# Performance work log

Measured on AMD Instinct MI355X. Metric: run time of the kernel, lower is better.

## Reference

```python
import jax, jax.numpy as jnp
import numpy as np

KSIZE = 7
FEAT_SIZE = 64
BETA = 0.02


def _resize_bilinear_ac(x, out_h, out_w):
    """Bilinear resize with align_corners=True. x: (B, C, H, W)."""
    H, W = x.shape[-2], x.shape[-1]
    ys = jnp.linspace(0.0, H - 1.0, out_h)
    xs = jnp.linspace(0.0, W - 1.0, out_w)
    y0 = jnp.clip(jnp.floor(ys).astype(jnp.int32), 0, H - 1)
    x0 = jnp.clip(jnp.floor(xs).astype(jnp.int32), 0, W - 1)
    y1 = jnp.minimum(y0 + 1, H - 1)
    x1 = jnp.minimum(x0 + 1, W - 1)
    wy = (ys - y0.astype(x.dtype))[None, None, :, None]
    wx = (xs - x0.astype(x.dtype))[None, None, None, :]
    rows = x[:, :, y0, :] * (1.0 - wy) + x[:, :, y1, :] * wy      # (B,C,out_h,W)
    out = rows[:, :, :, x0] * (1.0 - wx) + rows[:, :, :, x1] * wx  # (B,C,out_h,out_w)
    return out


def _sce(feat, w, b):
    """EfficientSpatialContextNet: shifted local-correlation context + 1x1 conv + relu."""
    B, C, h, wd = feat.shape
    k, pad = KSIZE, KSIZE // 2
    # F.normalize(p=2, dim=1) with eps=1e-12 (clamped norm)
    fn = feat / jnp.maximum(jnp.sqrt(jnp.sum(feat * feat, axis=1, keepdims=True)), 1e-12)
    fp = jnp.pad(fn, ((0, 0), (0, 0), (pad, pad), (pad, pad)))
    offsets = ([(i, i) for i in range(k)]
               + [(i, pad) for i in range(k)]
               + [(i, k - 1 - i) for i in range(k)]
               + [(pad, i) for i in range(k)])
    ctx = jnp.stack([jnp.sum(fp[:, :, r:h + r, c:wd + c] * fn, axis=1)
                     for (r, c) in offsets], axis=1)  # (B, 4k, h, w)
    out = jnp.concatenate([feat, ctx], axis=1)        # (B, C+4k, h, w)
    out = jnp.einsum('oc,bchw->bohw', w, out) + b[None, :, None, None]
    return jax.nn.relu(out)


def _l2norm(f):
    # FeatureL2Norm: eps added inside sqrt
    return f / jnp.sqrt(jnp.sum(f * f, axis=1, keepdims=True) + 1e-6)


def _forward(src_feat, tgt_feat, sce_w, sce_b):
    fs = FEAT_SIZE
    s = _l2norm(_sce(src_feat, sce_w, sce_b))
    t = _l2norm(_sce(tgt_feat, sce_w, sce_b))
    B, C, hs, ws = s.shape
    ht, wt = t.shape[2], t.shape[3]
    Ls, Lt = hs * ws, ht * wt
    corr = jnp.einsum('bcs,bct->bst', s.reshape(B, C, Ls), t.reshape(B, C, Lt))
    # mutual NN filter (Rocco et al.)
    smax = jnp.max(corr, axis=2, keepdims=True)
    tmax = jnp.max(corr, axis=1, keepdims=True)
    smax = jnp.where(smax == 0, 1e-30, smax)
    tmax = jnp.where(tmax == 0, 1e-30, tmax)
    corr = corr * ((corr / smax) * (corr / tmax))
    # resize corr on source grid, then on target grid (bilinear, align_corners=True)
    c_s2t = jnp.transpose(corr, (0, 2, 1)).reshape(B, Lt, hs, ws)
    c_s2t = _resize_bilinear_ac(c_s2t, fs, fs)                       # (B, Lt, fs, fs)
    c_t2s = jnp.transpose(c_s2t.reshape(B, Lt, fs * fs), (0, 2, 1)).reshape(B, fs * fs, ht, wt)
    c = _resize_bilinear_ac(c_t2s, fs, fs)                           # (B, fs*fs, fs, fs)
    # soft argmax with temperature (softmax over source positions)
    p = jax.nn.softmax(c / BETA, axis=1).reshape(B, fs, fs, fs, fs)  # (B, hs', ws', ht', wt')
    xn = jnp.linspace(-1.0, 1.0, fs).astype(c.dtype)
    yn = jnp.linspace(-1.0, 1.0, fs).astype(c.dtype)
    grid_x = jnp.einsum('bijhw,j->bhw', p, xn)
    grid_y = jnp.einsum('bijhw,i->bhw', p, yn)
    flow_norm = jnp.stack([grid_x, grid_y], axis=1)                  # (B, 2, fs, fs)
    # unnormalise mapping and convert to flow
    H = W = fs
    mx = (flow_norm[:, 0] + 1.0) * (W - 1) / 2.0
    my = (flow_norm[:, 1] + 1.0) * (H - 1) / 2.0
    xx = jnp.arange(W, dtype=flow_norm.dtype)[None, None, :]
    yy = jnp.arange(H, dtype=flow_norm.dtype)[None, :, None]
    flow = jnp.stack([mx - xx, my - yy], axis=1)                     # (B, 2, fs, fs)
    return flow


def setup_inputs() -> dict:
    key = jax.random.key(0)
    k1, k2, k3 = jax.random.split(key, 3)
    B, C, h, w = 4, 1024, 32, 32
    src_feat = jax.random.normal(k1, (B, C, h, w), dtype=jnp.float32)
    tgt_feat = jax.random.normal(k2, (B, C, h, w), dtype=jnp.float32)
    sce_w = jax.random.normal(k3, (2048, C + 4 * KSIZE), dtype=jnp.float32) * 0.03
    sce_b = jnp.zeros((2048,), dtype=jnp.float32)
    return {"src_feat": src_feat, "tgt_feat": tgt_feat, "sce_w": sce_w, "sce_b": sce_b}


def reference(src_feat, tgt_feat, sce_w, sce_b):
    return _forward(src_feat, tgt_feat, sce_w, sce_b)
```

## Files before the change

### kernel.cpp

```cpp
#include <hip/hip_runtime.h>
#include <math.h>

#define HW    1024
#define CIN   1024
#define CCTX  28
#define CALL  1052
#define COUT  2048
#define CCHNK 512

typedef _Float16 half8   __attribute__((ext_vector_type(8)));
typedef _Float16 half4_t __attribute__((ext_vector_type(4)));
typedef _Float16 half2_t __attribute__((ext_vector_type(2)));
typedef __fp16   fp16x2  __attribute__((ext_vector_type(2)));
typedef float    f32x4   __attribute__((ext_vector_type(4)));

__device__ __forceinline__ void split2(float a0, float a1, half2_t& h, half2_t& l) {
    float h0 = __uint_as_float(__float_as_uint(a0) & 0xFFFFE000u);
    float h1 = __uint_as_float(__float_as_uint(a1) & 0xFFFFE000u);
    fp16x2 hp = __builtin_amdgcn_cvt_pkrtz(h0, h1);
    fp16x2 lp = __builtin_amdgcn_cvt_pkrtz(a0 - h0, a1 - h1);
    h = __builtin_bit_cast(half2_t, hp);
    l = __builtin_bit_cast(half2_t, lp);
}
__device__ __forceinline__ void split4(float4 v, half4_t& h, half4_t& l) {
    half2_t ha, la, hb, lb;
    split2(v.x, v.y, ha, la);
    split2(v.z, v.w, hb, lb);
    h = __builtin_shufflevector(ha, hb, 0, 1, 2, 3);
    l = __builtin_shufflevector(la, lb, 0, 1, 2, 3);
}
__device__ __forceinline__ float f4get(const float4& v, int e) {
    return e == 0 ? v.x : e == 1 ? v.y : e == 2 ? v.z : v.w;
}

__global__ void pnorm_part(const float* __restrict__ src, const float* __restrict__ tgt,
                           float* __restrict__ parts) {
    int img = blockIdx.x, pb = blockIdx.y, part = blockIdx.z;
    int p = pb * 64 + threadIdx.x;
    const float* feat = ((img < 4) ? src + (size_t)img * CIN * HW
                                   : tgt + (size_t)(img - 4) * CIN * HW)
                        + (size_t)part * 256 * HW + p;
    float a4[4] = {};
    for (int c = 0; c < 256; c += 8) {
        float v[8];
#pragma unroll
        for (int j = 0; j < 8; ++j) v[j] = feat[(size_t)(c + j) * HW];
#pragma unroll
        for (int j = 0; j < 8; ++j) a4[j & 3] = fmaf(v[j], v[j], a4[j & 3]);
    }
    parts[(size_t)part * 8192 + img * 1024 + p] = (a4[0] + a4[1]) + (a4[2] + a4[3]);
}
__global__ void pnorm_combine(const float* __restrict__ parts, float* __restrict__ pnorm) {
    int img = blockIdx.x;
    int p = blockIdx.y * 64 + threadIdx.x;
    float s = parts[img * 1024 + p] + parts[8192 + img * 1024 + p]
            + parts[16384 + img * 1024 + p] + parts[24576 + img * 1024 + p];
    pnorm[img * HW + p] = fmaxf(sqrtf(s), 1e-12f);
}

__global__ void ctx_kernel(const float* __restrict__ src, const float* __restrict__ tgt,
                           const float* __restrict__ pnorm, float* __restrict__ ctx) {
    int img = blockIdx.x;
    int y = blockIdx.y;
    int tid = threadIdx.x;
    int o = tid >> 5;
    int x = tid & 31;
    const float* feat = (img < 4) ? src + (size_t)img * CIN * HW
                                  : tgt + (size_t)(img - 4) * CIN * HW;
    int g = o / 7, i = o % 7;
    int r, c;
    if (g == 0)      { r = i; c = i; }
    else if (g == 1) { r = i; c = 3; }
    else if (g == 2) { r = i; c = 6 - i; }
    else             { r = 3; c = i; }
    int y2 = y + r - 3, x2 = x + c - 3;
    int p = y * 32 + x;
    float outv = 0.f;
    if (y2 >= 0 && y2 < 32 && x2 >= 0 && x2 < 32) {
        int p2 = y2 * 32 + x2;
        const float* f0 = feat + p;
        const float* f1 = feat + p2;
        float acc = 0.f;
        for (int ch = 0; ch < CIN; ++ch)
            acc = fmaf(f0[(size_t)ch * HW], f1[(size_t)ch * HW], acc);
        outv = acc / (pnorm[img * HW + p] * pnorm[img * HW + p2]);
    }
    ctx[((size_t)img * CCTX + o) * HW + p] = outv;
}

template <bool FIRST>
__global__ __launch_bounds__(256) void conv_mfma(
    const float* __restrict__ src, const float* __restrict__ tgt,
    const float* __restrict__ ctxb, const float* __restrict__ w,
    const float* __restrict__ bias, _Float16* __restrict__ yh,
    _Float16* __restrict__ yl, float* __restrict__ nrm_parts, int c0) {
    __shared__ __align__(16) char smem[51200];
    _Float16* Ah = (_Float16*)smem;
    _Float16* Al = Ah + 2560;
    _Float16* Wh = Al + 2560;
    _Float16* Wl = Wh + 10240;

    int cb = blockIdx.x, pb = blockIdx.y, img = blockIdx.z;
    int n0 = pb * 64;
    int m0g = c0 + cb * 256;
    const float* feat = (img < 4) ? src + (size_t)img * CIN * HW
                                  : tgt + (size_t)(img - 4) * CIN * HW;
    const float* ctxi = ctxb + (size_t)img * CCTX * HW;
    int tid = threadIdx.x;
    int lane = tid & 63, wv = tid >> 6;
    int frow = lane & 15, kg = (lane >> 4) * 8;
    int aq = tid & 15, ar = tid >> 4;

    float4 xa[2], xw[8];
    auto stage_regs = [&](int k0) {
#pragma unroll
        for (int j = 0; j < 2; ++j) {
            int k = k0 + ar * 2 + j;
            if (k < CIN)       xa[j] = *(const float4*)(feat + (size_t)k * HW + n0 + aq * 4);
            else if (k < CALL) xa[j] = *(const float4*)(ctxi + (size_t)(k - CIN) * HW + n0 + aq * 4);
            else               xa[j] = make_float4(0.f, 0.f, 0.f, 0.f);
        }
#pragma unroll
        for (int i = 0; i < 8; ++i) {
            int k = k0 + i * 4;
            xw[i] = (k + 4 <= CALL) ? *(const float4*)(w + (size_t)(m0g + tid) * CALL + k)
                                    : make_float4(0.f, 0.f, 0.f, 0.f);
        }
    };
    auto write_lds = [&]() {
#pragma unroll
        for (int p = 0; p < 4; ++p) {
            half2_t h, l;
            split2(f4get(xa[0], p), f4get(xa[1], p), h, l);
            int row = aq * 4 + p;
            *(half2_t*)(Ah + row * 40 + ar * 2) = h;
            *(half2_t*)(Al + row * 40 + ar * 2) = l;
        }
#pragma unroll
        for (int i = 0; i < 8; ++i) {
            half4_t h, l;
            split4(xw[i], h, l);
            *(half4_t*)(Wh + tid * 40 + i * 4) = h;
            *(half4_t*)(Wl + tid * 40 + i * 4) = l;
        }
    };

    f32x4 acc[4][4] = {};
    const int NT = 33;
    stage_regs(0); write_lds();
    __syncthreads();
    for (int t = 0; t < NT; ++t) {
        half8 afh[4], afl[4], bfh[4], bfl[4];
#pragma unroll
        for (int fm = 0; fm < 4; ++fm) {
            int r = fm * 16 + frow;
            afh[fm] = *(const half8*)(Ah + r * 40 + kg);
            afl[fm] = *(const half8*)(Al + r * 40 + kg);
        }
#pragma unroll
        for (int fn = 0; fn < 4; ++fn) {
            int r = wv * 64 + fn * 16 + frow;
            bfh[fn] = *(const half8*)(Wh + r * 40 + kg);
            bfl[fn] = *(const half8*)(Wl + r * 40 + kg);
        }
        if (t + 1 < NT) stage_regs((t + 1) * 32);
#pragma unroll
        for (int fm = 0; fm < 4; ++fm)
#pragma unroll
            for (int fn = 0; fn < 4; ++fn) {
                acc[fm][fn] = __builtin_amdgcn_mfma_f32_16x16x32_f16(afh[fm], bfh[fn], acc[fm][fn], 0, 0, 0);
                acc[fm][fn] = __builtin_amdgcn_mfma_f32_16x16x32_f16(afh[fm], bfl[fn], acc[fm][fn], 0, 0, 0);
                acc[fm][fn] = __builtin_amdgcn_mfma_f32_16x16x32_f16(afl[fm], bfh[fn], acc[fm][fn], 0, 0, 0);
            }
        __syncthreads();
        if (t + 1 < NT) write_lds();
        __syncthreads();
    }

    float bv[4];
#pragma unroll
    for (int fn = 0; fn < 4; ++fn) bv[fn] = bias[m0g + wv * 64 + fn * 16 + frow];

    float* nsf = (float*)smem;
    _Float16* yb = (_Float16*)(smem + 2048);
    float psum[4][4] = {};
#pragma unroll
    for (int fm = 0; fm < 4; ++fm)
#pragma unroll
        for (int fn = 0; fn < 4; ++fn)
#pragma unroll
            for (int r = 0; r < 4; ++r) {
                float v = fmaxf(acc[fm][fn][r] + bv[fn], 0.f);
                acc[fm][fn][r] = v;
                psum[fm][r] = fmaf(v, v, psum[fm][r]);
            }
#pragma unroll
    for (int off = 1; off <= 8; off <<= 1)
#pragma unroll
        for (int fm = 0; fm < 4; ++fm)
#pragma unroll
            for (int r = 0; r < 4; ++r)
                psum[fm][r] = psum[fm][r] + __shfl_xor(psum[fm][r], off);
    if (frow == 0) {
#pragma unroll
        for (int fm = 0; fm < 4; ++fm)
#pragma unroll
            for (int r = 0; r < 4; ++r)
                nsf[wv * 64 + fm * 16 + (lane >> 4) * 4 + r] = psum[fm][r];
    }
    __syncthreads();
    float sv = 0.f;
    if (tid < 64)
        sv = nsf[tid] + nsf[64 + tid] + nsf[128 + tid] + nsf[192 + tid];
#pragma unroll
    for (int fm = 0; fm < 4; ++fm)
#pragma unroll
        for (int fn = 0; fn < 4; ++fn)
#pragma unroll
            for (int r = 0; r < 4; ++r) {
                float v = acc[fm][fn][r];
                float hf = __uint_as_float(__float_as_uint(v) & 0xFFFFE000u);
                int pix_l = fm * 16 + (lane >> 4) * 4 + r;
                int chan_l = wv * 64 + fn * 16 + frow;
                yb[pix_l * 264 + chan_l] = (_Float16)hf;
            }
    __syncthreads();
    {
        int row = tid >> 2, seg = tid & 3;
        _Float16* gp = yh + ((size_t)img * HW + n0 + row) * CCHNK + cb * 256 + seg * 64;
#pragma unroll
        for (int i = 0; i < 8; ++i)
            *(half8*)(gp + i * 8) = *(const half8*)(yb + row * 264 + seg * 64 + i * 8);
    }
    __syncthreads();
#pragma unroll
    for (int fm = 0; fm < 4; ++fm)
#pragma unroll
        for (int fn = 0; fn < 4; ++fn)
#pragma unroll
            for (int r = 0; r < 4; ++r) {
                float v = acc[fm][fn][r];
                float hf = __uint_as_float(__float_as_uint(v) & 0xFFFFE000u);
                int pix_l = fm * 16 + (lane >> 4) * 4 + r;
                int chan_l = wv * 64 + fn * 16 + frow;
                yb[pix_l * 264 + chan_l] = (_Float16)(v - hf);
            }
    __syncthreads();
    {
        int row = tid >> 2, seg = tid & 3;
        _Float16* gp = yl + ((size_t)img * HW + n0 + row) * CCHNK + cb * 256 + seg * 64;
#pragma unroll
        for (int i = 0; i < 8; ++i)
            *(half8*)(gp + i * 8) = *(const half8*)(yb + row * 264 + seg * 64 + i * 8);
    }
    if (tid < 64) {
        float* np = nrm_parts + ((size_t)img * 2 + cb) * HW + n0 + tid;
        if (FIRST) *np = sv; else *np += sv;
    }
}

template <int MODE>
__global__ __launch_bounds__(256) void corr_mfma(
    const _Float16* __restrict__ yh, const _Float16* __restrict__ yl,
    const float* __restrict__ nrm_sq, float* __restrict__ corrT,
    float* __restrict__ spar, float* __restrict__ tpar) {
    __shared__ float rm[2][128];
    __shared__ float cm[2][128];
    int sb = blockIdx.x, tb = blockIdx.y, b = blockIdx.z;
    int tid = threadIdx.x, lane = tid & 63, wv = tid >> 6;
    int wm = wv >> 1, wn = wv & 1;
    int frow = lane & 15, kg = (lane >> 4) * 8;

    size_t trow = (size_t)(4 + b) * HW + tb * 128 + wm * 64 + frow;
    size_t srow = (size_t)b * HW + sb * 128 + wn * 64 + frow;
    const _Float16* ahp = yh + trow * CCHNK + kg;
    const _Float16* alp = yl + trow * CCHNK + kg;
    const _Float16* bhp = yh + srow * CCHNK + kg;
    const _Float16* blp = yl + srow * CCHNK + kg;

    f32x4 acc[4][4] = {};
#pragma unroll 2
    for (int t = 0; t < 16; ++t) {
        int k0 = t * 32;
        half8 ah[4], al_[4], bh[4], bl[4];
#pragma unroll
        for (int f = 0; f < 4; ++f) {
            size_t ro = (size_t)f * 16 * CCHNK + k0;
            ah[f]  = *(const half8*)(ahp + ro);
            al_[f] = *(const half8*)(alp + ro);
            bh[f]  = *(const half8*)(bhp + ro);
            bl[f]  = *(const half8*)(blp + ro);
        }
#pragma unroll
        for (int fm = 0; fm < 4; ++fm)
#pragma unroll
            for (int fn = 0; fn < 4; ++fn) {
                acc[fm][fn] = __builtin_amdgcn_mfma_f32_16x16x32_f16(ah[fm],  bh[fn], acc[fm][fn], 0, 0, 0);
                acc[fm][fn] = __builtin_amdgcn_mfma_f32_16x16x32_f16(ah[fm],  bl[fn], acc[fm][fn], 0, 0, 0);
                acc[fm][fn] = __builtin_amdgcn_mfma_f32_16x16x32_f16(al_[fm], bh[fn], acc[fm][fn], 0, 0, 0);
            }
    }

    float rnt[4][4], rns[4];
    float rowmax[4][4] = {};
    float colmax[4] = {};
    if (MODE == 2) {
#pragma unroll
        for (int fm = 0; fm < 4; ++fm)
#pragma unroll
            for (int r = 0; r < 4; ++r) {
                int t = tb * 128 + wm * 64 + fm * 16 + (lane >> 4) * 4 + r;
                rnt[fm][r] = 1.f / sqrtf(nrm_sq[(size_t)(4 + b) * HW + t] + 1e-6f);
            }
#pragma unroll
        for (int fn = 0; fn < 4; ++fn) {
            int s_ = sb * 128 + wn * 64 + fn * 16 + frow;
            rns[fn] = 1.f / sqrtf(nrm_sq[(size_t)b * HW + s_] + 1e-6f);
        }
    }
#pragma unroll
    for (int fm = 0; fm < 4; ++fm)
#pragma unroll
        for (int r = 0; r < 4; ++r) {
            int t = tb * 128 + wm * 64 + fm * 16 + (lane >> 4) * 4 + r;
            float* cp = corrT + ((size_t)b * HW + t) * HW + sb * 128 + wn * 64 + frow;
#pragma unroll
            for (int fn = 0; fn < 4; ++fn) {
                float v = acc[fm][fn][r];
                if (MODE >= 1) v += cp[fn * 16];
                if (MODE == 2) {
                    v *= rnt[fm][r] * rns[fn];
                    rowmax[fm][r] = fmaxf(rowmax[fm][r], v);
                    colmax[fn] = fmaxf(colmax[fn], v);
                }
                cp[fn * 16] = v;
            }
        }
    if (MODE == 2) {
#pragma unroll
        for (int off = 1; off <= 8; off <<= 1)
#pragma unroll
            for (int fm = 0; fm < 4; ++fm)
#pragma unroll
                for (int r = 0; r < 4; ++r)
                    rowmax[fm][r] = fmaxf(rowmax[fm][r], __shfl_xor(rowmax[fm][r], off));
        if (frow == 0) {
#pragma unroll
            for (int fm = 0; fm < 4; ++fm)
#pragma unroll
                for (int r = 0; r < 4; ++r)
                    rm[wn][wm * 64 + fm * 16 + (lane >> 4) * 4 + r] = rowmax[fm][r];
        }
#pragma unroll
        for (int off = 16; off <= 32; off <<= 1)
#pragma unroll
            for (int fn = 0; fn < 4; ++fn)
                colmax[fn] = fmaxf(colmax[fn], __shfl_xor(colmax[fn], off));
        if (lane < 16) {
#pragma unroll
            for (int fn = 0; fn < 4; ++fn)
                cm[wm][wn * 64 + fn * 16 + lane] = colmax[fn];
        }
        __syncthreads();
        if (tid < 128)
            tpar[((size_t)b * 8 + sb) * HW + tb * 128 + tid] = fmaxf(rm[0][tid], rm[1][tid]);
        if (tid < 128)
            spar[((size_t)b * 8 + tb) * HW + sb * 128 + tid] = fmaxf(cm[0][tid], cm[1][tid]);
    }
}

__global__ void nrm_reduce(const float* __restrict__ nrm_parts, float* __restrict__ nrm_sq) {
    int img = blockIdx.y;
    int p = blockIdx.x * 256 + threadIdx.x;
    nrm_sq[img * HW + p] = nrm_parts[((size_t)img * 2 + 0) * HW + p]
                         + nrm_parts[((size_t)img * 2 + 1) * HW + p];
}

__global__ void combine_max(const float* __restrict__ spar, const float* __restrict__ tpar,
                            float* __restrict__ smax, float* __restrict__ tmax) {
    int b = blockIdx.y;
    int i = blockIdx.x * 256 + threadIdx.x;
    float m = 0.f;
#pragma unroll
    for (int q = 0; q < 8; ++q) m = fmaxf(m, spar[((size_t)b * 8 + q) * HW + i]);
    smax[b * HW + i] = m;
    float m2 = 0.f;
#pragma unroll
    for (int q = 0; q < 8; ++q) m2 = fmaxf(m2, tpar[((size_t)b * 8 + q) * HW + i]);
    tmax[b * HW + i] = m2;
}

__global__ __launch_bounds__(256) void final_kernel(const float* __restrict__ corrT,
                                                    const float* __restrict__ smax,
                                                    const float* __restrict__ tmax,
                                                    float* __restrict__ out) {
    __shared__ float vsh[1024];
    __shared__ float rbuf[16];
    int b = blockIdx.z;
    int typ = blockIdx.y;
    int txp = blockIdx.x;
    int tid = threadIdx.x;

    float fy = typ * (31.0f / 63.0f);
    int y0 = min((int)fy, 31); int y1 = min(y0 + 1, 31);
    float wy = fy - (float)y0;
    float fx = txp * (31.0f / 63.0f);
    int x0 = min((int)fx, 31); int x1 = min(x0 + 1, 31);
    float wx = fx - (float)x0;
    int tA = y0 * 32 + x0, tB = y0 * 32 + x1, tC = y1 * 32 + x0, tD = y1 * 32 + x1;
    const float* base = corrT + (size_t)b * HW * HW;
    const float* rA = base + (size_t)tA * HW;
    const float* rB = base + (size_t)tB * HW;
    const float* rC = base + (size_t)tC * HW;
    const float* rD = base + (size_t)tD * HW;
    float tmA_ = tmax[b * HW + tA]; if (tmA_ == 0.f) tmA_ = 1e-30f;
    float tmB_ = tmax[b * HW + tB]; if (tmB_ == 0.f) tmB_ = 1e-30f;
    float tmC_ = tmax[b * HW + tC]; if (tmC_ == 0.f) tmC_ = 1e-30f;
    float tmD_ = tmax[b * HW + tD]; if (tmD_ == 0.f) tmD_ = 1e-30f;
    float itA = 1.f / tmA_, itB = 1.f / tmB_, itC = 1.f / tmC_, itD = 1.f / tmD_;
    float wA = (1.f - wy) * (1.f - wx), wB = (1.f - wy) * wx;
    float wC = wy * (1.f - wx), wD = wy * wx;
#pragma unroll
    for (int u = 0; u < 4; ++u) {
        int s = u * 256 + tid;
        float sm = smax[b * HW + s]; if (sm == 0.f) sm = 1e-30f;
        float is = 1.f / sm;
        float a = rA[s]; a = a * a * a * is * itA;
        float b2 = rB[s]; b2 = b2 * b2 * b2 * is * itB;
        float c2 = rC[s]; c2 = c2 * c2 * c2 * is * itC;
        float d2 = rD[s]; d2 = d2 * d2 * d2 * is * itD;
        vsh[s] = wA * a + wB * b2 + wC * c2 + wD * d2;
    }
    __syncthreads();

    int jx = tid & 63;
    int wvq = tid >> 6;
    float gxx = jx * (31.0f / 63.0f);
    int sx0 = min((int)gxx, 31), sx1 = min(sx0 + 1, 31);
    float wxx = gxx - (float)sx0, iwxx = 1.f - wxx;
    float xnj = jx * (2.0f / 63.0f) - 1.0f;

    float cv[16];
    float lmax = -1e30f;
#pragma unroll
    for (int u = 0; u < 16; ++u) {
        int iy = u * 4 + wvq;
        float gy = iy * (31.0f / 63.0f);
        int sy0 = min((int)gy, 31), sy1 = min(sy0 + 1, 31);
        float wyy = gy - (float)sy0;
        float r0 = vsh[sy0 * 32 + sx0] * iwxx + vsh[sy0 * 32 + sx1] * wxx;
        float r1 = vsh[sy1 * 32 + sx0] * iwxx + vsh[sy1 * 32 + sx1] * wxx;
        cv[u] = (r0 * (1.f - wyy) + r1 * wyy) * 50.0f;
        lmax = fmaxf(lmax, cv[u]);
    }
#pragma unroll
    for (int off = 32; off >= 1; off >>= 1) lmax = fmaxf(lmax, __shfl_down(lmax, off));
    int lane = tid & 63;
    if (lane == 0) rbuf[wvq] = lmax;
    __syncthreads();
    if (tid == 0) {
        float m = rbuf[0];
        for (int i = 1; i < 4; ++i) m = fmaxf(m, rbuf[i]);
        rbuf[0] = m;
    }
    __syncthreads();
    float m = rbuf[0];

    float e0 = 0.f, ex = 0.f, ey = 0.f;
#pragma unroll
    for (int u = 0; u < 16; ++u) {
        int iy = u * 4 + wvq;
        float e = __expf(cv[u] - m);
        e0 += e;
        ex = fmaf(e, xnj, ex);
        ey = fmaf(e, iy * (2.0f / 63.0f) - 1.0f, ey);
    }
#pragma unroll
    for (int off = 32; off >= 1; off >>= 1) {
        e0 += __shfl_down(e0, off);
        ex += __shfl_down(ex, off);
        ey += __shfl_down(ey, off);
    }
    if (lane == 0) { rbuf[4 + wvq] = e0; rbuf[8 + wvq] = ex; rbuf[12 + wvq] = ey; }
    __syncthreads();
    if (tid == 0) {
        float s0 = rbuf[4] + rbuf[5] + rbuf[6] + rbuf[7];
        float sx = rbuf[8] + rbuf[9] + rbuf[10] + rbuf[11];
        float sy = rbuf[12] + rbuf[13] + rbuf[14] + rbuf[15];
        float gx = sx / s0, gy = sy / s0;
        float mx = (gx + 1.f) * 31.5f;
        float my = (gy + 1.f) * 31.5f;
        out[(((size_t)b * 2 + 0) * 64 + typ) * 64 + txp] = mx - (float)txp;
        out[(((size_t)b * 2 + 1) * 64 + typ) * 64 + txp] = my - (float)typ;
    }
}

extern "C" void kernel_launch(void* const* d_in, const int* in_sizes, int n_in,
                              void* d_out, int out_size, void* d_ws, size_t ws_size,
                              hipStream_t stream) {
    const float* src  = (const float*)d_in[0];
    const float* tgt  = (const float*)d_in[1];
    const float* sw   = (const float*)d_in[2];
    const float* sb   = (const float*)d_in[3];
    float* out = (float*)d_out;

    float* f = (float*)d_ws;
    float*     corrT     = f;
    _Float16*  yh        = (_Float16*)(f + 4194304);
    _Float16*  yl        = (_Float16*)(f + 4194304 + 2097152);
    float*     nrm_parts = f + 8388608;
    float*     tpar      = nrm_parts + 16384;
    float*     nrm_sq    = tpar + 32768;
    float*     smax      = nrm_sq + 8192;
    float*     spar      = smax + 4096;
    float*     tmax      = spar + 32768;
    float*     pnorm     = tmax + 4096;
    float*     ctxbuf    = pnorm + 8192;
    float*     pparts    = (float*)yh;

    pnorm_part<<<dim3(8, 16, 4), 64, 0, stream>>>(src, tgt, pparts);
    pnorm_combine<<<dim3(8, 16), 64, 0, stream>>>(pparts, pnorm);
    ctx_kernel<<<dim3(8, 32), 896, 0, stream>>>(src, tgt, pnorm, ctxbuf);

    conv_mfma<true><<<dim3(2, 16, 8), 256, 0, stream>>>(src, tgt, ctxbuf, sw, sb,
                                                        yh, yl, nrm_parts, 0);
    corr_mfma<0><<<dim3(8, 8, 4), 256, 0, stream>>>(yh, yl, nrm_sq, corrT, spar, tpar);
    for (int c = 1; c < 3; ++c) {
        conv_mfma<false><<<dim3(2, 16, 8), 256, 0, stream>>>(src, tgt, ctxbuf, sw, sb,
                                                             yh, yl, nrm_parts, c * CCHNK);
        corr_mfma<1><<<dim3(8, 8, 4), 256, 0, stream>>>(yh, yl, nrm_sq, corrT, spar, tpar);
    }
    conv_mfma<false><<<dim3(2, 16, 8), 256, 0, stream>>>(src, tgt, ctxbuf, sw, sb,
                                                         yh, yl, nrm_parts, 3 * CCHNK);
    nrm_reduce<<<dim3(4, 8), 256, 0, stream>>>(nrm_parts, nrm_sq);
    corr_mfma<2><<<dim3(8, 8, 4), 256, 0, stream>>>(yh, yl, nrm_sq, corrT, spar, tpar);

    combine_max<<<dim3(4, 4), 256, 0, stream>>>(spar, tpar, smax, tmax);
    final_kernel<<<dim3(64, 64, 4), 256, 0, stream>>>(corrT, smax, tmax, out);
}
```

Before: 633.5 us.

## Split ctx reduction over channels, shrink conv/corr tiles, double-buffer conv LDS

The channel reduction in the context-correlation kernel is split into 8 channel slices that write partial sums, and a separate combine kernel applies the normalisation. The conv GEMM now uses 128-channel output tiles with a k-major LDS layout, double buffering and one barrier per step. The corr GEMM becomes a single-wave block with 64x32 tiles, writing row and column max partials straight to global memory. Together these aim to fill the 256 CUs with more blocks, at the cost of extra kernel launches, more partial-max traffic and less data reuse per block.

```diff
diff --git a/kernel.cpp b/kernel.cpp
--- a/kernel.cpp
+++ b/kernel.cpp
@@ -31,6 +31,13 @@
 }
 __device__ __forceinline__ float f4get(const float4& v, int e) {
     return e == 0 ? v.x : e == 1 ? v.y : e == 2 ? v.z : v.w;
+}
+__device__ __forceinline__ void ctx_offset(int o, int& r, int& c) {
+    int g = o / 7, i = o % 7;
+    if (g == 0)      { r = i; c = i; }
+    else if (g == 1) { r = i; c = 3; }
+    else if (g == 2) { r = i; c = 6 - i; }
+    else             { r = 3; c = i; }
 }
 
 __global__ void pnorm_part(const float* __restrict__ src, const float* __restrict__ tgt,
@@ -58,60 +65,65 @@
     pnorm[img * HW + p] = fmaxf(sqrtf(s), 1e-12f);
 }
 
-__global__ void ctx_kernel(const float* __restrict__ src, const float* __restrict__ tgt,
-                           const float* __restrict__ pnorm, float* __restrict__ ctx) {
-    int img = blockIdx.x;
-    int y = blockIdx.y;
+__global__ void ctx_part(const float* __restrict__ src, const float* __restrict__ tgt,
+                         float* __restrict__ ctxpar) {
+    int img = blockIdx.x, y = blockIdx.y, part = blockIdx.z;
     int tid = threadIdx.x;
-    int o = tid >> 5;
-    int x = tid & 31;
-    const float* feat = (img < 4) ? src + (size_t)img * CIN * HW
-                                  : tgt + (size_t)(img - 4) * CIN * HW;
-    int g = o / 7, i = o % 7;
-    int r, c;
-    if (g == 0)      { r = i; c = i; }
-    else if (g == 1) { r = i; c = 3; }
-    else if (g == 2) { r = i; c = 6 - i; }
-    else             { r = 3; c = i; }
+    int o = tid >> 5, x = tid & 31;
+    const float* feat = ((img < 4) ? src + (size_t)img * CIN * HW
+                                   : tgt + (size_t)(img - 4) * CIN * HW)
+                        + (size_t)part * 128 * HW;
+    int r, c; ctx_offset(o, r, c);
     int y2 = y + r - 3, x2 = x + c - 3;
     int p = y * 32 + x;
-    float outv = 0.f;
+    float acc = 0.f;
     if (y2 >= 0 && y2 < 32 && x2 >= 0 && x2 < 32) {
         int p2 = y2 * 32 + x2;
         const float* f0 = feat + p;
         const float* f1 = feat + p2;
-        float acc = 0.f;
-        for (int ch = 0; ch < CIN; ++ch)
+        for (int ch = 0; ch < 128; ++ch)
             acc = fmaf(f0[(size_t)ch * HW], f1[(size_t)ch * HW], acc);
-        outv = acc / (pnorm[img * HW + p] * pnorm[img * HW + p2]);
-    }
-    ctx[((size_t)img * CCTX + o) * HW + p] = outv;
+    }
+    ctxpar[((size_t)part * 8 + img) * 28672 + o * 1024 + p] = acc;
+}
+__global__ void ctx_combine(const float* __restrict__ ctxpar, const float* __restrict__ pnorm,
+                            float* __restrict__ ctxbuf) {
+    int o = blockIdx.y, img = blockIdx.z;
+    int p = blockIdx.x * 256 + threadIdx.x;
+    float s = 0.f;
+#pragma unroll
+    for (int part = 0; part < 8; ++part)
+        s += ctxpar[((size_t)part * 8 + img) * 28672 + o * 1024 + p];
+    int r, c; ctx_offset(o, r, c);
+    int y = p >> 5, x = p & 31;
+    int y2 = y + r - 3, x2 = x + c - 3;
+    bool inb = (y2 >= 0 && y2 < 32 && x2 >= 0 && x2 < 32);
+    int p2 = inb ? y2 * 32 + x2 : p;
+    float outv = s / (pnorm[img * HW + p] * pnorm[img * HW + p2]);
+    ctxbuf[((size_t)img * CCTX + o) * 1024 + p] = outv;
 }
 
 template <bool FIRST>
-__global__ __launch_bounds__(256) void conv_mfma(
+__global__ __launch_bounds__(256, 2) void conv_mfma(
     const float* __restrict__ src, const float* __restrict__ tgt,
     const float* __restrict__ ctxb, const float* __restrict__ w,
     const float* __restrict__ bias, _Float16* __restrict__ yh,
     _Float16* __restrict__ yl, float* __restrict__ nrm_parts, int c0) {
-    __shared__ __align__(16) char smem[51200];
-    _Float16* Ah = (_Float16*)smem;
-    _Float16* Al = Ah + 2560;
-    _Float16* Wh = Al + 2560;
-    _Float16* Wl = Wh + 10240;
+    __shared__ __align__(16) _Float16 lds[2 * 12288];
 
     int cb = blockIdx.x, pb = blockIdx.y, img = blockIdx.z;
     int n0 = pb * 64;
-    int m0g = c0 + cb * 256;
+    int m0g = c0 + cb * 128;
     const float* feat = (img < 4) ? src + (size_t)img * CIN * HW
                                   : tgt + (size_t)(img - 4) * CIN * HW;
     const float* ctxi = ctxb + (size_t)img * CCTX * HW;
     int tid = threadIdx.x;
     int lane = tid & 63, wv = tid >> 6;
-    int frow = lane & 15, kg = (lane >> 4) * 8;
+    int frow = lane & 15, kp = lane >> 4;
     int aq = tid & 15, ar = tid >> 4;
-
-    float4 xa[2], xw[8];
+    int wrow = tid >> 1, wh_ = tid & 1;
+
+    float4 xa[2], xw[4];
     auto stage_regs = [&](int k0) {
 #pragma unroll
         for (int j = 0; j < 2; ++j) {
@@ -121,73 +133,79 @@
             else               xa[j] = make_float4(0.f, 0.f, 0.f, 0.f);
         }
 #pragma unroll
-        for (int i = 0; i < 8; ++i) {
-            int k = k0 + i * 4;
-            xw[i] = (k + 4 <= CALL) ? *(const float4*)(w + (size_t)(m0g + tid) * CALL + k)
+        for (int i = 0; i < 4; ++i) {
+            int k = k0 + wh_ * 16 + i * 4;
+            xw[i] = (k + 4 <= CALL) ? *(const float4*)(w + (size_t)(m0g + wrow) * CALL + k)
                                     : make_float4(0.f, 0.f, 0.f, 0.f);
         }
     };
-    auto write_lds = [&]() {
+    auto write_lds = [&](int buf) {
+        _Float16* B = lds + buf * 12288;
+        int xkp = ar >> 2, xoff = (ar & 3) * 2;
 #pragma unroll
         for (int p = 0; p < 4; ++p) {
             half2_t h, l;
             split2(f4get(xa[0], p), f4get(xa[1], p), h, l);
-            int row = aq * 4 + p;
-            *(half2_t*)(Ah + row * 40 + ar * 2) = h;
-            *(half2_t*)(Al + row * 40 + ar * 2) = l;
-        }
-#pragma unroll
-        for (int i = 0; i < 8; ++i) {
-            half4_t h, l;
-            split4(xw[i], h, l);
-            *(half4_t*)(Wh + tid * 40 + i * 4) = h;
-            *(half4_t*)(Wl + tid * 40 + i * 4) = l;
+            int idx = xkp * 512 + (aq * 4 + p) * 8 + xoff;
+            *(half2_t*)(B + idx) = h;
+            *(half2_t*)(B + 2048 + idx) = l;
+        }
+#pragma unroll
+        for (int i2 = 0; i2 < 2; ++i2) {
+            half4_t h0, l0, h1, l1;
+            split4(xw[2 * i2], h0, l0);
+            split4(xw[2 * i2 + 1], h1, l1);
+            half8 hh = __builtin_shufflevector(h0, h1, 0, 1, 2, 3, 4, 5, 6, 7);
+            half8 ll = __builtin_shufflevector(l0, l1, 0, 1, 2, 3, 4, 5, 6, 7);
+            int idx = (wh_ * 2 + i2) * 1024 + wrow * 8;
+            *(half8*)(B + 4096 + idx) = hh;
+            *(half8*)(B + 8192 + idx) = ll;
         }
     };
 
-    f32x4 acc[4][4] = {};
+    f32x4 acc[4][2] = {};
     const int NT = 33;
-    stage_regs(0); write_lds();
+    stage_regs(0); write_lds(0);
     __syncthreads();
     for (int t = 0; t < NT; ++t) {
-        half8 afh[4], afl[4], bfh[4], bfl[4];
+        const _Float16* Bc = lds + (t & 1) * 12288;
+        half8 afh[4], afl[4], bfh[2], bfl[2];
 #pragma unroll
         for (int fm = 0; fm < 4; ++fm) {
-            int r = fm * 16 + frow;
-            afh[fm] = *(const half8*)(Ah + r * 40 + kg);
-            afl[fm] = *(const half8*)(Al + r * 40 + kg);
-        }
-#pragma unroll
-        for (int fn = 0; fn < 4; ++fn) {
-            int r = wv * 64 + fn * 16 + frow;
-            bfh[fn] = *(const half8*)(Wh + r * 40 + kg);
-            bfl[fn] = *(const half8*)(Wl + r * 40 + kg);
+            int idx = kp * 512 + (fm * 16 + frow) * 8;
+            afh[fm] = *(const half8*)(Bc + idx);
+            afl[fm] = *(const half8*)(Bc + 2048 + idx);
+        }
+#pragma unroll
+        for (int fn = 0; fn < 2; ++fn) {
+            int idx = kp * 1024 + (wv * 32 + fn * 16 + frow) * 8;
+            bfh[fn] = *(const half8*)(Bc + 4096 + idx);
+            bfl[fn] = *(const half8*)(Bc + 8192 + idx);
         }
         if (t + 1 < NT) stage_regs((t + 1) * 32);
 #pragma unroll
         for (int fm = 0; fm < 4; ++fm)
 #pragma unroll
-            for (int fn = 0; fn < 4; ++fn) {
+            for (int fn = 0; fn < 2; ++fn) {
                 acc[fm][fn] = __builtin_amdgcn_mfma_f32_16x16x32_f16(afh[fm], bfh[fn], acc[fm][fn], 0, 0, 0);
                 acc[fm][fn] = __builtin_amdgcn_mfma_f32_16x16x32_f16(afh[fm], bfl[fn], acc[fm][fn], 0, 0, 0);
                 acc[fm][fn] = __builtin_amdgcn_mfma_f32_16x16x32_f16(afl[fm], bfh[fn], acc[fm][fn], 0, 0, 0);
             }
+        if (t + 1 < NT) write_lds((t + 1) & 1);
         __syncthreads();
-        if (t + 1 < NT) write_lds();
-        __syncthreads();
-    }
-
-    float bv[4];
-#pragma unroll
-    for (int fn = 0; fn < 4; ++fn) bv[fn] = bias[m0g + wv * 64 + fn * 16 + frow];
-
-    float* nsf = (float*)smem;
-    _Float16* yb = (_Float16*)(smem + 2048);
+    }
+
+    float bv[2];
+#pragma unroll
+    for (int fn = 0; fn < 2; ++fn) bv[fn] = bias[m0g + wv * 32 + fn * 16 + frow];
+
+    float* nsf = (float*)lds;
+    _Float16* yb = lds + 512;
     float psum[4][4] = {};
 #pragma unroll
     for (int fm = 0; fm < 4; ++fm)
 #pragma unroll
-        for (int fn = 0; fn < 4; ++fn)
+        for (int fn = 0; fn < 2; ++fn)
 #pragma unroll
             for (int r = 0; r < 4; ++r) {
                 float v = fmaxf(acc[fm][fn][r] + bv[fn], 0.f);
@@ -206,115 +224,117 @@
         for (int fm = 0; fm < 4; ++fm)
 #pragma unroll
             for (int r = 0; r < 4; ++r)
-                nsf[wv * 64 + fm * 16 + (lane >> 4) * 4 + r] = psum[fm][r];
+                nsf[wv * 64 + fm * 16 + kp * 4 + r] = psum[fm][r];
     }
     __syncthreads();
     float sv = 0.f;
     if (tid < 64)
         sv = nsf[tid] + nsf[64 + tid] + nsf[128 + tid] + nsf[192 + tid];
+    __syncthreads();
 #pragma unroll
     for (int fm = 0; fm < 4; ++fm)
 #pragma unroll
-        for (int fn = 0; fn < 4; ++fn)
+        for (int fn = 0; fn < 2; ++fn)
 #pragma unroll
             for (int r = 0; r < 4; ++r) {
                 float v = acc[fm][fn][r];
                 float hf = __uint_as_float(__float_as_uint(v) & 0xFFFFE000u);
-                int pix_l = fm * 16 + (lane >> 4) * 4 + r;
-                int chan_l = wv * 64 + fn * 16 + frow;
-                yb[pix_l * 264 + chan_l] = (_Float16)hf;
+                int pix_l = fm * 16 + kp * 4 + r;
+                int chan_l = wv * 32 + fn * 16 + frow;
+                yb[pix_l * 136 + chan_l] = (_Float16)hf;
             }
     __syncthreads();
     {
         int row = tid >> 2, seg = tid & 3;
-        _Float16* gp = yh + ((size_t)img * HW + n0 + row) * CCHNK + cb * 256 + seg * 64;
-#pragma unroll
-        for (int i = 0; i < 8; ++i)
-            *(half8*)(gp + i * 8) = *(const half8*)(yb + row * 264 + seg * 64 + i * 8);
+        _Float16* gp = yh + ((size_t)img * HW + n0 + row) * CCHNK + cb * 128 + seg * 32;
+#pragma unroll
+        for (int i = 0; i < 4; ++i)
+            *(half8*)(gp + i * 8) = *(const half8*)(yb + row * 136 + seg * 32 + i * 8);
     }
     __syncthreads();
 #pragma unroll
     for (int fm = 0; fm < 4; ++fm)
 #pragma unroll
-        for (int fn = 0; fn < 4; ++fn)
+        for (int fn = 0; fn < 2; ++fn)
 #pragma unroll
             for (int r = 0; r < 4; ++r) {
                 float v = acc[fm][fn][r];
                 float hf = __uint_as_float(__float_as_uint(v) & 0xFFFFE000u);
-                int pix_l = fm * 16 + (lane >> 4) * 4 + r;
-                int chan_l = wv * 64 + fn * 16 + frow;
-                yb[pix_l * 264 + chan_l] = (_Float16)(v - hf);
+                int pix_l = fm * 16 + kp * 4 + r;
+                int chan_l = wv * 32 + fn * 16 + frow;
+                yb[pix_l * 136 + chan_l] = (_Float16)(v - hf);
             }
     __syncthreads();
     {
         int row = tid >> 2, seg = tid & 3;
-        _Float16* gp = yl + ((size_t)img * HW + n0 + row) * CCHNK + cb * 256 + seg * 64;
-#pragma unroll
-        for (int i = 0; i < 8; ++i)
-            *(half8*)(gp + i * 8) = *(const half8*)(yb + row * 264 + seg * 64 + i * 8);
+        _Float16* gp = yl + ((size_t)img * HW + n0 + row) * CCHNK + cb * 128 + seg * 32;
+#pragma unroll
+        for (int i = 0; i < 4; ++i)
+            *(half8*)(gp + i * 8) = *(const half8*)(yb + row * 136 + seg * 32 + i * 8);
     }
     if (tid < 64) {
-        float* np = nrm_parts + ((size_t)img * 2 + cb) * HW + n0 + tid;
+        float* np = nrm_parts + ((size_t)img * 4 + cb) * HW + n0 + tid;
         if (FIRST) *np = sv; else *np += sv;
     }
 }
 
 template <int MODE>
-__global__ __launch_bounds__(256) void corr_mfma(
+__global__ __launch_bounds__(64) void corr_mfma(
     const _Float16* __restrict__ yh, const _Float16* __restrict__ yl,
     const float* __restrict__ nrm_sq, float* __restrict__ corrT,
     float* __restrict__ spar, float* __restrict__ tpar) {
-    __shared__ float rm[2][128];
-    __shared__ float cm[2][128];
     int sb = blockIdx.x, tb = blockIdx.y, b = blockIdx.z;
-    int tid = threadIdx.x, lane = tid & 63, wv = tid >> 6;
-    int wm = wv >> 1, wn = wv & 1;
-    int frow = lane & 15, kg = (lane >> 4) * 8;
-
-    size_t trow = (size_t)(4 + b) * HW + tb * 128 + wm * 64 + frow;
-    size_t srow = (size_t)b * HW + sb * 128 + wn * 64 + frow;
-    const _Float16* ahp = yh + trow * CCHNK + kg;
-    const _Float16* alp = yl + trow * CCHNK + kg;
-    const _Float16* bhp = yh + srow * CCHNK + kg;
-    const _Float16* blp = yl + srow * CCHNK + kg;
-
-    f32x4 acc[4][4] = {};
-#pragma unroll 2
+    int lane = threadIdx.x;
+    int frow = lane & 15, kp = lane >> 4;
+
+    size_t trow = (size_t)(4 + b) * HW + tb * 64 + frow;
+    size_t srow = (size_t)b * HW + sb * 32 + frow;
+    const _Float16* ahp = yh + trow * CCHNK + kp * 8;
+    const _Float16* alp = yl + trow * CCHNK + kp * 8;
+    const _Float16* bhp = yh + srow * CCHNK + kp * 8;
+    const _Float16* blp = yl + srow * CCHNK + kp * 8;
+
+    f32x4 acc[4][2] = {};
+#pragma unroll 4
     for (int t = 0; t < 16; ++t) {
         int k0 = t * 32;
-        half8 ah[4], al_[4], bh[4], bl[4];
-#pragma unroll
-        for (int f = 0; f < 4; ++f) {
-            size_t ro = (size_t)f * 16 * CCHNK + k0;
-            ah[f]  = *(const half8*)(ahp + ro);
-            al_[f] = *(const half8*)(alp + ro);
-            bh[f]  = *(const half8*)(bhp + ro);
-            bl[f]  = *(const half8*)(blp + ro);
+        half8 ah[4], al_[4], bh[2], bl[2];
+#pragma unroll
+        for (int fm = 0; fm < 4; ++fm) {
+            size_t ro = (size_t)fm * 16 * CCHNK + k0;
+            ah[fm]  = *(const half8*)(ahp + ro);
+            al_[fm] = *(const half8*)(alp + ro);
+        }
+#pragma unroll
+        for (int fn = 0; fn < 2; ++fn) {
+            size_t ro = (size_t)fn * 16 * CCHNK + k0;
+            bh[fn] = *(const half8*)(bhp + ro);
+            bl[fn] = *(const half8*)(blp + ro);
         }
 #pragma unroll
         for (int fm = 0; fm < 4; ++fm)
 #pragma unroll
-            for (int fn = 0; fn < 4; ++fn) {
+            for (int fn = 0; fn < 2; ++fn) {
                 acc[fm][fn] = __builtin_amdgcn_mfma_f32_16x16x32_f16(ah[fm],  bh[fn], acc[fm][fn], 0, 0, 0);
                 acc[fm][fn] = __builtin_amdgcn_mfma_f32_16x16x32_f16(ah[fm],  bl[fn], acc[fm][fn], 0, 0, 0);
                 acc[fm][fn] = __builtin_amdgcn_mfma_f32_16x16x32_f16(al_[fm], bh[fn], acc[fm][fn], 0, 0, 0);
             }
     }
 
-    float rnt[4][4], rns[4];
+    float rnt[4][4], rns[2];
     float rowmax[4][4] = {};
-    float colmax[4] = {};
+    float colmax[2] = {0.f, 0.f};
     if (MODE == 2) {
 #pragma unroll
         for (int fm = 0; fm < 4; ++fm)
 #pragma unroll
             for (int r = 0; r < 4; ++r) {
-                int t = tb * 128 + wm * 64 + fm * 16 + (lane >> 4) * 4 + r;
+                int t = tb * 64 + fm * 16 + kp * 4 + r;
                 rnt[fm][r] = 1.f / sqrtf(nrm_sq[(size_t)(4 + b) * HW + t] + 1e-6f);
             }
 #pragma unroll
-        for (int fn = 0; fn < 4; ++fn) {
-            int s_ = sb * 128 + wn * 64 + fn * 16 + frow;
+        for (int fn = 0; fn < 2; ++fn) {
+            int s_ = sb * 32 + fn * 16 + frow;
             rns[fn] = 1.f / sqrtf(nrm_sq[(size_t)b * HW + s_] + 1e-6f);
         }
     }
@@ -322,10 +342,10 @@
     for (int fm = 0; fm < 4; ++fm)
 #pragma unroll
         for (int r = 0; r < 4; ++r) {
-            int t = tb * 128 + wm * 64 + fm * 16 + (lane >> 4) * 4 + r;
-            float* cp = corrT + ((size_t)b * HW + t) * HW + sb * 128 + wn * 64 + frow;
-#pragma unroll
-            for (int fn = 0; fn < 4; ++fn) {
+            int t = tb * 64 + fm * 16 + kp * 4 + r;
+            float* cp = corrT + ((size_t)b * HW + t) * HW + sb * 32 + frow;
+#pragma unroll
+            for (int fn = 0; fn < 2; ++fn) {
                 float v = acc[fm][fn][r];
                 if (MODE >= 1) v += cp[fn * 16];
                 if (MODE == 2) {
@@ -349,31 +369,29 @@
             for (int fm = 0; fm < 4; ++fm)
 #pragma unroll
                 for (int r = 0; r < 4; ++r)
-                    rm[wn][wm * 64 + fm * 16 + (lane >> 4) * 4 + r] = rowmax[fm][r];
+                    tpar[((size_t)b * 32 + sb) * HW + tb * 64 + fm * 16 + kp * 4 + r] = rowmax[fm][r];
         }
 #pragma unroll
         for (int off = 16; off <= 32; off <<= 1)
 #pragma unroll
-            for (int fn = 0; fn < 4; ++fn)
+            for (int fn = 0; fn < 2; ++fn)
                 colmax[fn] = fmaxf(colmax[fn], __shfl_xor(colmax[fn], off));
-        if (lane < 16) {
-#pragma unroll
-            for (int fn = 0; fn < 4; ++fn)
-                cm[wm][wn * 64 + fn * 16 + lane] = colmax[fn];
-        }
-        __syncthreads();
-        if (tid < 128)
-            tpar[((size_t)b * 8 + sb) * HW + tb * 128 + tid] = fmaxf(rm[0][tid], rm[1][tid]);
-        if (tid < 128)
-            spar[((size_t)b * 8 + tb) * HW + sb * 128 + tid] = fmaxf(cm[0][tid], cm[1][tid]);
+        if (kp == 0) {
+#pragma unroll
+            for (int fn = 0; fn < 2; ++fn)
+                spar[((size_t)b * 16 + tb) * HW + sb * 32 + fn * 16 + lane] = colmax[fn];
+        }
     }
 }
 
 __global__ void nrm_reduce(const float* __restrict__ nrm_parts, float* __restrict__ nrm_sq) {
     int img = blockIdx.y;
     int p = blockIdx.x * 256 + threadIdx.x;
-    nrm_sq[img * HW + p] = nrm_parts[((size_t)img * 2 + 0) * HW + p]
-                         + nrm_parts[((size_t)img * 2 + 1) * HW + p];
+    float s = 0.f;
+#pragma unroll
+    for (int mb = 0; mb < 4; ++mb)
+        s += nrm_parts[((size_t)img * 4 + mb) * HW + p];
+    nrm_sq[img * HW + p] = s;
 }
 
 __global__ void combine_max(const float* __restrict__ spar, const float* __restrict__ tpar,
@@ -382,11 +400,11 @@
     int i = blockIdx.x * 256 + threadIdx.x;
     float m = 0.f;
 #pragma unroll
-    for (int q = 0; q < 8; ++q) m = fmaxf(m, spar[((size_t)b * 8 + q) * HW + i]);
+    for (int q = 0; q < 16; ++q) m = fmaxf(m, spar[((size_t)b * 16 + q) * HW + i]);
     smax[b * HW + i] = m;
     float m2 = 0.f;
 #pragma unroll
-    for (int q = 0; q < 8; ++q) m2 = fmaxf(m2, tpar[((size_t)b * 8 + q) * HW + i]);
+    for (int q = 0; q < 32; ++q) m2 = fmaxf(m2, tpar[((size_t)b * 32 + q) * HW + i]);
     tmax[b * HW + i] = m2;
 }
 
@@ -507,33 +525,35 @@
     float* f = (float*)d_ws;
     float*     corrT     = f;
     _Float16*  yh        = (_Float16*)(f + 4194304);
-    _Float16*  yl        = (_Float16*)(f + 4194304 + 2097152);
+    _Float16*  yl        = (_Float16*)(f + 6291456);
     float*     nrm_parts = f + 8388608;
-    float*     tpar      = nrm_parts + 16384;
-    float*     nrm_sq    = tpar + 32768;
+    float*     nrm_sq    = nrm_parts + 32768;
     float*     smax      = nrm_sq + 8192;
-    float*     spar      = smax + 4096;
-    float*     tmax      = spar + 32768;
+    float*     tmax      = smax + 4096;
     float*     pnorm     = tmax + 4096;
     float*     ctxbuf    = pnorm + 8192;
+    float*     ctxpar    = corrT;
     float*     pparts    = (float*)yh;
+    float*     tpar      = ctxbuf;
+    float*     spar      = ctxbuf + 131072;
 
     pnorm_part<<<dim3(8, 16, 4), 64, 0, stream>>>(src, tgt, pparts);
     pnorm_combine<<<dim3(8, 16), 64, 0, stream>>>(pparts, pnorm);
-    ctx_kernel<<<dim3(8, 32), 896, 0, stream>>>(src, tgt, pnorm, ctxbuf);
-
-    conv_mfma<true><<<dim3(2, 16, 8), 256, 0, stream>>>(src, tgt, ctxbuf, sw, sb,
+    ctx_part<<<dim3(8, 32, 8), 896, 0, stream>>>(src, tgt, ctxpar);
+    ctx_combine<<<dim3(4, 28, 8), 256, 0, stream>>>(ctxpar, pnorm, ctxbuf);
+
+    conv_mfma<true><<<dim3(4, 16, 8), 256, 0, stream>>>(src, tgt, ctxbuf, sw, sb,
                                                         yh, yl, nrm_parts, 0);
-    corr_mfma<0><<<dim3(8, 8, 4), 256, 0, stream>>>(yh, yl, nrm_sq, corrT, spar, tpar);
+    corr_mfma<0><<<dim3(32, 16, 4), 64, 0, stream>>>(yh, yl, nrm_sq, corrT, spar, tpar);
     for (int c = 1; c < 3; ++c) {
-        conv_mfma<false><<<dim3(2, 16, 8), 256, 0, stream>>>(src, tgt, ctxbuf, sw, sb,
+        conv_mfma<false><<<dim3(4, 16, 8), 256, 0, stream>>>(src, tgt, ctxbuf, sw, sb,
                                                              yh, yl, nrm_parts, c * CCHNK);
-        corr_mfma<1><<<dim3(8, 8, 4), 256, 0, stream>>>(yh, yl, nrm_sq, corrT, spar, tpar);
-    }
-    conv_mfma<false><<<dim3(2, 16, 8), 256, 0, stream>>>(src, tgt, ctxbuf, sw, sb,
+        corr_mfma<1><<<dim3(32, 16, 4), 64, 0, stream>>>(yh, yl, nrm_sq, corrT, spar, tpar);
+    }
+    conv_mfma<false><<<dim3(4, 16, 8), 256, 0, stream>>>(src, tgt, ctxbuf, sw, sb,
                                                          yh, yl, nrm_parts, 3 * CCHNK);
     nrm_reduce<<<dim3(4, 8), 256, 0, stream>>>(nrm_parts, nrm_sq);
-    corr_mfma<2><<<dim3(8, 8, 4), 256, 0, stream>>>(yh, yl, nrm_sq, corrT, spar, tpar);
+    corr_mfma<2><<<dim3(32, 16, 4), 64, 0, stream>>>(yh, yl, nrm_sq, corrT, spar, tpar);
 
     combine_max<<<dim3(4, 4), 256, 0, stream>>>(spar, tpar, smax, tmax);
     final_kernel<<<dim3(64, 64, 4), 256, 0, stream>>>(corrT, smax, tmax, out);
```

Result: faster. 608.2 us (-4.0%).
